# Optimization experiments

Measured on AMD Instinct MI355X. Metric: run time of the kernel, lower is better.

Reference implementation:

```python
import jax, jax.numpy as jnp
import numpy as np

NEG_INF = -1e30


def setup_inputs() -> dict:
    key = jax.random.key(0)
    ks = jax.random.split(key, 11)
    b, n, d = 4, 2048, 1024
    scale = 1.0 / np.sqrt(d)
    inp = {
        "q": jax.random.normal(ks[0], (b, n, d), jnp.float32),
        "k": jax.random.normal(ks[1], (b, n, d), jnp.float32),
        "v": jax.random.normal(ks[2], (b, n, d), jnp.float32),
        # nn.Linear params: weight [out, in], bias [out]
        "Wq": jax.random.normal(ks[3], (d, d), jnp.float32) * scale,
        "bq": jnp.zeros((d,), jnp.float32),
        "Wk": jax.random.normal(ks[4], (d, d), jnp.float32) * scale,
        "bk": jnp.zeros((d,), jnp.float32),
        "Wv": jax.random.normal(ks[5], (d, d), jnp.float32) * scale,
        "bv": jnp.zeros((d,), jnp.float32),
        "Wo": jax.random.normal(ks[6], (d, d), jnp.float32) * scale,
        "bo": jnp.zeros((d,), jnp.float32),
    }
    return inp


def reference(q, k, v, Wq, bq, Wk, bk, Wv, bv, Wo, bo):
    # Faithful to source: the multi-head reshape/transpose results are never
    # assigned, so attention runs single-headed over full n_embd vectors.
    b, n, d = q.shape
    qp = q @ Wq.T + bq  # [b, n, d]
    kp = k @ Wk.T + bk
    vp = v @ Wv.T + bv
    scale = jnp.asarray(1.0 / d, qp.dtype) ** 0.5  # sqrt(1/d)
    att = jnp.einsum('bnd,bmd->bnm', qp, kp) * scale  # [b, n, n]
    causal = jnp.tril(jnp.ones((n, n), bool))          # block_size tril sliced to n
    att = jnp.where(causal[None, :, :], att, NEG_INF)
    att = jax.nn.softmax(att, axis=-1)  # dropout p=0.0 -> identity
    y = att @ vp                        # [b, n, d]
    # source bug reproduced: transpose(1,2) then reshape(b, n, d)
    y = jnp.swapaxes(y, 1, 2).reshape(b, n, d)
    y = y @ Wo.T + bo
    return y
```

## Files before the change

### kernel.cpp

```cpp
#include <hip/hip_runtime.h>
#include <hip/hip_bf16.h>
#include <stdint.h>

typedef __bf16 bf16_t;
typedef __bf16 bf16x8 __attribute__((ext_vector_type(8)));
typedef __bf16 bf16x4 __attribute__((ext_vector_type(4)));
typedef float f32x4 __attribute__((ext_vector_type(4)));

#define GLD_LDS16(src, dst)                                                              \
  __builtin_amdgcn_global_load_lds((const __attribute__((address_space(1))) void*)(src), \
                                   (__attribute__((address_space(3))) void*)(dst), 16, 0, 0)

struct CvtArgs {
  const float* src[7];
  bf16_t* dst[7];
  long n4[7];
};

__global__ __launch_bounds__(256) void cvt_all(CvtArgs a) {
  const int seg = blockIdx.y;
  const float* __restrict__ in = a.src[seg];
  bf16_t* __restrict__ out = a.dst[seg];
  const long n4 = a.n4[seg];
  long i = (long)blockIdx.x * blockDim.x + threadIdx.x;
  const long stride = (long)gridDim.x * blockDim.x;
  for (; i < n4; i += stride) {
    float4 v = ((const float4*)in)[i];
    bf16x4 o;
    o[0] = (bf16_t)v.x; o[1] = (bf16_t)v.y; o[2] = (bf16_t)v.z; o[3] = (bf16_t)v.w;
    ((bf16x4*)out)[i] = o;
  }
}

__global__ __launch_bounds__(256) void softmax_causal(bf16_t* __restrict__ S, int n, long sB) {
  const int i = blockIdx.x;
  const int z = blockIdx.y;
  bf16_t* row = S + (long)z * sB + (long)i * n;
  const int t = threadIdx.x;
  const int j0 = t << 3;
  const int jmax = ((i >> 7) + 1) << 7;
  const bool active = j0 < jmax;

  float vals[8];
  float mx = -3.0e38f;
  if (active) {
    bf16x8 vv = ((const bf16x8*)row)[t];
#pragma unroll
    for (int e = 0; e < 8; ++e) {
      float v = (j0 + e <= i) ? (float)vv[e] : -3.0e38f;
      vals[e] = v;
      mx = fmaxf(mx, v);
    }
  }
#pragma unroll
  for (int off = 32; off; off >>= 1) mx = fmaxf(mx, __shfl_xor(mx, off));
  __shared__ float redm[4];
  if ((t & 63) == 0) redm[t >> 6] = mx;
  __syncthreads();
  mx = fmaxf(fmaxf(redm[0], redm[1]), fmaxf(redm[2], redm[3]));

  float sum = 0.f;
  if (active) {
#pragma unroll
    for (int e = 0; e < 8; ++e) {
      float p = (j0 + e <= i) ? __expf(vals[e] - mx) : 0.f;
      vals[e] = p;
      sum += p;
    }
  }
#pragma unroll
  for (int off = 32; off; off >>= 1) sum += __shfl_xor(sum, off);
  __shared__ float reds[4];
  if ((t & 63) == 0) reds[t >> 6] = sum;
  __syncthreads();
  sum = reds[0] + reds[1] + reds[2] + reds[3];
  const float inv = 1.0f / sum;

  if (active) {
    bf16x8 o;
#pragma unroll
    for (int e = 0; e < 8; ++e) o[e] = (bf16_t)(vals[e] * inv);
    ((bf16x8*)row)[t] = o;
  }
}

__device__ __forceinline__ void xcd_remap(int& bx, int& by, int& bz) {
  const int gx = gridDim.x, gy = gridDim.y;
  int lin = (blockIdx.z * gy + blockIdx.y) * gx + blockIdx.x;
  const int nwg = gx * gy * (int)gridDim.z;
  lin = (lin & 7) * (nwg >> 3) + (lin >> 3);
  bx = lin % gx;
  const int rem = lin / gx;
  by = rem % gy;
  bz = rem / gy;
}

template <int NF>
__device__ __forceinline__ void gemm_core(char* smem,
                                          const bf16_t* __restrict__ A,
                                          const bf16_t* __restrict__ B,
                                          int K, int KT, int m0, int n0,
                                          f32x4 (&acc)[4][NF]) {
  char* const asb = smem;
  char* const bsb = smem + 16384;
  const int t = threadIdx.x;
  const int l = t & 63;
  const int w = t >> 6;
  const int wr = w >> 1, wc = w & 1;
  const int r16 = l & 15, kg = l >> 4;

  const bf16_t* a_src[4];
  const bf16_t* b_src[NF];
#pragma unroll
  for (int i = 0; i < 4; ++i) {
    const int c = i * 256 + t;
    const int row = c >> 3;
    const int sl = (c & 7) ^ (row & 7);
    a_src[i] = A + (long)(m0 + row) * K + sl * 8;
  }
#pragma unroll
  for (int i = 0; i < NF; ++i) {
    const int c = i * 256 + t;
    const int row = c >> 3;
    const int sl = (c & 7) ^ (row & 7);
    b_src[i] = B + (long)(n0 + row) * K + sl * 8;
  }

  int aoff[2][4], boff[2][NF];
#pragma unroll
  for (int kp = 0; kp < 2; ++kp) {
#pragma unroll
    for (int mi = 0; mi < 4; ++mi) {
      const int ra = wr * 64 + mi * 16 + r16;
      aoff[kp][mi] = ra * 128 + ((kp * 4 + kg) ^ (ra & 7)) * 16;
    }
#pragma unroll
    for (int ni = 0; ni < NF; ++ni) {
      const int rb = wc * (NF * 16) + ni * 16 + r16;
      boff[kp][ni] = rb * 128 + ((kp * 4 + kg) ^ (rb & 7)) * 16;
    }
  }

  for (int kt = 0; kt < KT; ++kt) {
    __syncthreads();
#pragma unroll
    for (int i = 0; i < 4; ++i) {
      GLD_LDS16(a_src[i], asb + i * 4096 + w * 1024);
      a_src[i] += 64;
    }
#pragma unroll
    for (int i = 0; i < NF; ++i) {
      GLD_LDS16(b_src[i], bsb + i * 4096 + w * 1024);
      b_src[i] += 64;
    }
    __syncthreads();

#pragma unroll
    for (int kp = 0; kp < 2; ++kp) {
      bf16x8 af[4], bfr[NF];
#pragma unroll
      for (int mi = 0; mi < 4; ++mi) af[mi] = *(const bf16x8*)(asb + aoff[kp][mi]);
#pragma unroll
      for (int ni = 0; ni < NF; ++ni) bfr[ni] = *(const bf16x8*)(bsb + boff[kp][ni]);
#pragma unroll
      for (int mi = 0; mi < 4; ++mi)
#pragma unroll
        for (int ni = 0; ni < NF; ++ni)
          acc[mi][ni] =
              __builtin_amdgcn_mfma_f32_16x16x32_bf16(af[mi], bfr[ni], acc[mi][ni], 0, 0, 0);
    }
  }
}

template <int NF, int EPI, bool BIAS, bool KBOUND>
__global__ __launch_bounds__(256, 4) void gemm_bt(const bf16_t* __restrict__ Ag,
                                                  const bf16_t* __restrict__ Bg,
                                                  const float* __restrict__ bias,
                                                  void* __restrict__ Cout,
                                                  int N, int K, float alpha,
                                                  long sAb, long sBb, long sCb, int eltC) {
  int bx, by, bz;
  xcd_remap(bx, by, bz);
  const int m0 = by << 7, n0 = bx * (NF * 32);

  int KT = K >> 6;
  if (KBOUND) {
    const int kb = (n0 + NF * 32) >> 6;
    if (kb < KT) KT = kb;
  }

  __shared__ __align__(16) char smem[16384 + NF * 4096];
  f32x4 acc[4][NF] = {};
  gemm_core<NF>(smem, Ag + (long)bz * sAb, Bg + (long)bz * sBb, K, KT, m0, n0, acc);

  const int t = threadIdx.x;
  const int l = t & 63;
  const int w = t >> 6;
  const int wr = w >> 1, wc = w & 1;
  const int rowbase = m0 + wr * 64 + ((l >> 4) << 2);
  const int colbase = n0 + wc * (NF * 16) + (l & 15);
  if constexpr (EPI == 0) {
    float* C = (float*)((char*)Cout + (long)bz * sCb * eltC);
#pragma unroll
    for (int mi = 0; mi < 4; ++mi)
#pragma unroll
      for (int ni = 0; ni < NF; ++ni) {
        const int col = colbase + ni * 16;
        float badd = 0.f;
        if constexpr (BIAS) badd = bias[col];
#pragma unroll
        for (int j = 0; j < 4; ++j)
          C[(long)(rowbase + mi * 16 + j) * N + col] = acc[mi][ni][j] * alpha + badd;
      }
  } else {
    bf16_t* C = (bf16_t*)((char*)Cout + (long)bz * sCb * eltC);
#pragma unroll
    for (int mi = 0; mi < 4; ++mi)
#pragma unroll
      for (int ni = 0; ni < NF; ++ni) {
        const int col = colbase + ni * 16;
        float badd = 0.f;
        if constexpr (BIAS) badd = bias[col];
#pragma unroll
        for (int j = 0; j < 4; ++j)
          C[(long)(rowbase + mi * 16 + j) * N + col] = (bf16_t)(acc[mi][ni][j] * alpha + badd);
      }
  }
}

__global__ __launch_bounds__(256, 4) void gemm_scores(const bf16_t* __restrict__ qp,
                                                      const bf16_t* __restrict__ kp,
                                                      bf16_t* __restrict__ S,
                                                      long nd, long nn) {
  int bx, by, bz;
  xcd_remap(bx, by, bz);
  int r, c;
  if (bx <= 2 * by + 1) { r = by; c = bx; }
  else { r = 15 - by; c = bx + 15 - 2 * by; }
  const int m0 = r << 7, n0 = c << 6;

  __shared__ __align__(16) char smem[24576];
  f32x4 acc[4][2] = {};
  gemm_core<2>(smem, qp + (long)bz * nd, kp + (long)bz * nd, 1024, 16, m0, n0, acc);

  const int t = threadIdx.x;
  const int l = t & 63;
  const int w = t >> 6;
  const int wr = w >> 1, wc = w & 1;
  const int rowbase = m0 + wr * 64 + ((l >> 4) << 2);
  const int colbase = n0 + wc * 32 + (l & 15);
  bf16_t* C = S + (long)bz * nn;
#pragma unroll
  for (int mi = 0; mi < 4; ++mi)
#pragma unroll
    for (int ni = 0; ni < 2; ++ni) {
      const int col = colbase + ni * 16;
#pragma unroll
      for (int j = 0; j < 4; ++j)
        C[(long)(rowbase + mi * 16 + j) * 2048 + col] = (bf16_t)(acc[mi][ni][j] * 0.03125f);
    }
}

struct Qkv3Args {
  const bf16_t* A[3];
  const bf16_t* W[3];
  const float* bias[3];
  bf16_t* C[3];
};

__global__ __launch_bounds__(256, 4) void qkv3(Qkv3Args ga, int N, int K) {
  int bx, by, bz;
  xcd_remap(bx, by, bz);
  const int m0 = by << 7, n0 = bx << 7;

  __shared__ __align__(16) char smem[32768];
  f32x4 acc[4][4] = {};
  gemm_core<4>(smem, ga.A[bz], ga.W[bz], K, K >> 6, m0, n0, acc);

  const float* __restrict__ bias = ga.bias[bz];
  const int t = threadIdx.x;
  const int l = t & 63;
  const int w = t >> 6;
  const int wr = w >> 1, wc = w & 1;
  const int r16 = l & 15, kg = l >> 4;

  if (bz < 2) {
    bf16_t* C = ga.C[bz];
    const int rowbase = m0 + wr * 64 + kg * 4;
    const int colbase = n0 + wc * 64 + r16;
#pragma unroll
    for (int mi = 0; mi < 4; ++mi)
#pragma unroll
      for (int ni = 0; ni < 4; ++ni) {
        const int col = colbase + ni * 16;
        const float badd = bias[col];
#pragma unroll
        for (int j = 0; j < 4; ++j)
          C[(long)(rowbase + mi * 16 + j) * N + col] = (bf16_t)(acc[mi][ni][j] + badd);
      }
  } else {
    __syncthreads();
    char* tt = smem;
#pragma unroll
    for (int mi = 0; mi < 4; ++mi)
#pragma unroll
      for (int ni = 0; ni < 4; ++ni) {
        const int lc = wc * 64 + ni * 16 + r16;
        const int lrb = (wr * 64 + mi * 16 + kg * 4) * 2;
        const float badd = bias[n0 + lc];
        bf16x4 o;
#pragma unroll
        for (int j = 0; j < 4; ++j) o[j] = (bf16_t)(acc[mi][ni][j] + badd);
        *(bf16x4*)(tt + lc * 256 + (lrb ^ ((lc & 7) << 4))) = o;
      }
    __syncthreads();
    bf16_t* C = ga.C[2];
    const int batch = m0 >> 11, nb = m0 & 2047;
#pragma unroll
    for (int i = 0; i < 8; ++i) {
      const int c = i * 256 + t;
      const int lc = c >> 4, ch = c & 15;
      *(bf16x8*)(C + (long)batch * (2048 * 1024) + (long)(n0 + lc) * 2048 + nb + ch * 8) =
          *(const bf16x8*)(tt + lc * 256 + ((ch * 16) ^ ((lc & 7) << 4)));
    }
  }
}

extern "C" void kernel_launch(void* const* d_in, const int* in_sizes, int n_in,
                              void* d_out, int out_size, void* d_ws, size_t ws_size,
                              hipStream_t stream) {
  const int b = 4, n = 2048, d = 1024;
  const long nd  = (long)n * d;
  const long bn  = (long)b * n;
  const long bnd = bn * d;
  const long ddl = (long)d * d;
  const long nn  = (long)n * n;

  const float* q  = (const float*)d_in[0];
  const float* k  = (const float*)d_in[1];
  const float* v  = (const float*)d_in[2];
  const float* Wq = (const float*)d_in[3];
  const float* bq = (const float*)d_in[4];
  const float* Wk = (const float*)d_in[5];
  const float* bk = (const float*)d_in[6];
  const float* Wv = (const float*)d_in[7];
  const float* bv = (const float*)d_in[8];
  const float* Wo = (const float*)d_in[9];
  const float* bo = (const float*)d_in[10];

  bf16_t* ws  = (bf16_t*)d_ws;
  bf16_t* qB  = ws;
  bf16_t* kB  = qB + bnd;
  bf16_t* vB  = kB + bnd;
  bf16_t* WqB = vB + bnd;
  bf16_t* WkB = WqB + ddl;
  bf16_t* WvB = WkB + ddl;
  bf16_t* WoB = WvB + ddl;
  bf16_t* qpB = WoB + ddl;
  bf16_t* kpB = qpB + bnd;
  bf16_t* vpT = kpB + bnd;
  bf16_t* S   = vpT + bnd;
  bf16_t* yT  = S + (long)b * nn;
  const size_t need = (size_t)(7 * bnd + 4 * ddl + (long)b * nn) * 2;
  if (ws_size < need) return;

  dim3 blk(256);

  CvtArgs ca;
  ca.src[0] = q;  ca.dst[0] = qB;  ca.n4[0] = bnd / 4;
  ca.src[1] = k;  ca.dst[1] = kB;  ca.n4[1] = bnd / 4;
  ca.src[2] = v;  ca.dst[2] = vB;  ca.n4[2] = bnd / 4;
  ca.src[3] = Wq; ca.dst[3] = WqB; ca.n4[3] = ddl / 4;
  ca.src[4] = Wk; ca.dst[4] = WkB; ca.n4[4] = ddl / 4;
  ca.src[5] = Wv; ca.dst[5] = WvB; ca.n4[5] = ddl / 4;
  ca.src[6] = Wo; ca.dst[6] = WoB; ca.n4[6] = ddl / 4;
  cvt_all<<<dim3(512, 7), blk, 0, stream>>>(ca);

  Qkv3Args qa;
  qa.A[0] = qB; qa.W[0] = WqB; qa.bias[0] = bq; qa.C[0] = qpB;
  qa.A[1] = kB; qa.W[1] = WkB; qa.bias[1] = bk; qa.C[1] = kpB;
  qa.A[2] = vB; qa.W[2] = WvB; qa.bias[2] = bv; qa.C[2] = vpT;
  qkv3<<<dim3(d / 128, bn / 128, 3), blk, 0, stream>>>(qa, d, d);

  gemm_scores<<<dim3(17, 16, b), blk, 0, stream>>>(qpB, kpB, S, nd, nn);

  softmax_causal<<<dim3(n, b), blk, 0, stream>>>(S, n, nn);

  gemm_bt<2, 1, false, true><<<dim3(n / 64, d / 128, b), blk, 0, stream>>>(
      vpT, S, nullptr, yT, n, n, 1.f, nd, nn, nd, 2);

  gemm_bt<2, 0, true, false><<<dim3(d / 64, bn / 128, 1), blk, 0, stream>>>(
      yT, WoB, bo, (float*)d_out, d, d, 1.f, 0, 0, 0, 4);
}
```

Baseline: 181.3 us.

## Switch GEMM core from 16x16x32 to 32x32x16 bf16 MFMA tiles

Reworks the shared GEMM core and every epilogue to use 32x32x16 MFMA instructions with 16-wide f32 accumulators in place of 16x16x32 with 4-wide ones. Tile sizes per block stay the same but fragment offsets, LDS read patterns and output index mapping are rewritten. Larger MFMA tiles need fewer LDS fragment reads per FLOP and fewer instructions issued. The cost is longer per-instruction latency, a different register-pressure profile, and a write pattern where each lane stores rows spaced 8 apart.

```diff
diff --git a/kernel.cpp b/kernel.cpp
--- a/kernel.cpp
+++ b/kernel.cpp
@@ -6,6 +6,7 @@
 typedef __bf16 bf16x8 __attribute__((ext_vector_type(8)));
 typedef __bf16 bf16x4 __attribute__((ext_vector_type(4)));
 typedef float f32x4 __attribute__((ext_vector_type(4)));
+typedef float f32x16 __attribute__((ext_vector_type(16)));
 
 #define GLD_LDS16(src, dst)                                                              \
   __builtin_amdgcn_global_load_lds((const __attribute__((address_space(1))) void*)(src), \
@@ -95,22 +96,22 @@
   bz = rem / gy;
 }
 
-template <int NF>
+template <int NS>
 __device__ __forceinline__ void gemm_core(char* smem,
                                           const bf16_t* __restrict__ A,
                                           const bf16_t* __restrict__ B,
                                           int K, int KT, int m0, int n0,
-                                          f32x4 (&acc)[4][NF]) {
+                                          f32x16 (&acc)[2][NS]) {
   char* const asb = smem;
   char* const bsb = smem + 16384;
   const int t = threadIdx.x;
   const int l = t & 63;
   const int w = t >> 6;
   const int wr = w >> 1, wc = w & 1;
-  const int r16 = l & 15, kg = l >> 4;
+  const int l31 = l & 31, hi = l >> 5;
 
   const bf16_t* a_src[4];
-  const bf16_t* b_src[NF];
+  const bf16_t* b_src[NS * 2];
 #pragma unroll
   for (int i = 0; i < 4; ++i) {
     const int c = i * 256 + t;
@@ -119,25 +120,25 @@
     a_src[i] = A + (long)(m0 + row) * K + sl * 8;
   }
 #pragma unroll
-  for (int i = 0; i < NF; ++i) {
+  for (int i = 0; i < NS * 2; ++i) {
     const int c = i * 256 + t;
     const int row = c >> 3;
     const int sl = (c & 7) ^ (row & 7);
     b_src[i] = B + (long)(n0 + row) * K + sl * 8;
   }
 
-  int aoff[2][4], boff[2][NF];
-#pragma unroll
-  for (int kp = 0; kp < 2; ++kp) {
-#pragma unroll
-    for (int mi = 0; mi < 4; ++mi) {
-      const int ra = wr * 64 + mi * 16 + r16;
-      aoff[kp][mi] = ra * 128 + ((kp * 4 + kg) ^ (ra & 7)) * 16;
-    }
-#pragma unroll
-    for (int ni = 0; ni < NF; ++ni) {
-      const int rb = wc * (NF * 16) + ni * 16 + r16;
-      boff[kp][ni] = rb * 128 + ((kp * 4 + kg) ^ (rb & 7)) * 16;
+  int aoff[4][2], boff[4][NS];
+#pragma unroll
+  for (int kt = 0; kt < 4; ++kt) {
+#pragma unroll
+    for (int mi = 0; mi < 2; ++mi) {
+      const int ra = wr * 64 + mi * 32 + l31;
+      aoff[kt][mi] = ra * 128 + ((kt * 2 + hi) ^ (ra & 7)) * 16;
+    }
+#pragma unroll
+    for (int ni = 0; ni < NS; ++ni) {
+      const int rb = wc * (NS * 32) + ni * 32 + l31;
+      boff[kt][ni] = rb * 128 + ((kt * 2 + hi) ^ (rb & 7)) * 16;
     }
   }
 
@@ -149,30 +150,30 @@
       a_src[i] += 64;
     }
 #pragma unroll
-    for (int i = 0; i < NF; ++i) {
+    for (int i = 0; i < NS * 2; ++i) {
       GLD_LDS16(b_src[i], bsb + i * 4096 + w * 1024);
       b_src[i] += 64;
     }
     __syncthreads();
 
 #pragma unroll
-    for (int kp = 0; kp < 2; ++kp) {
-      bf16x8 af[4], bfr[NF];
-#pragma unroll
-      for (int mi = 0; mi < 4; ++mi) af[mi] = *(const bf16x8*)(asb + aoff[kp][mi]);
-#pragma unroll
-      for (int ni = 0; ni < NF; ++ni) bfr[ni] = *(const bf16x8*)(bsb + boff[kp][ni]);
-#pragma unroll
-      for (int mi = 0; mi < 4; ++mi)
-#pragma unroll
-        for (int ni = 0; ni < NF; ++ni)
+    for (int ks = 0; ks < 4; ++ks) {
+      bf16x8 af[2], bfr[NS];
+#pragma unroll
+      for (int mi = 0; mi < 2; ++mi) af[mi] = *(const bf16x8*)(asb + aoff[ks][mi]);
+#pragma unroll
+      for (int ni = 0; ni < NS; ++ni) bfr[ni] = *(const bf16x8*)(bsb + boff[ks][ni]);
+#pragma unroll
+      for (int mi = 0; mi < 2; ++mi)
+#pragma unroll
+        for (int ni = 0; ni < NS; ++ni)
           acc[mi][ni] =
-              __builtin_amdgcn_mfma_f32_16x16x32_bf16(af[mi], bfr[ni], acc[mi][ni], 0, 0, 0);
-    }
-  }
-}
-
-template <int NF, int EPI, bool BIAS, bool KBOUND>
+              __builtin_amdgcn_mfma_f32_32x32x16_bf16(af[mi], bfr[ni], acc[mi][ni], 0, 0, 0);
+    }
+  }
+}
+
+template <int NS, int EPI, bool BIAS, bool KBOUND>
 __global__ __launch_bounds__(256, 4) void gemm_bt(const bf16_t* __restrict__ Ag,
                                                   const bf16_t* __restrict__ Bg,
                                                   const float* __restrict__ bias,
@@ -181,49 +182,56 @@
                                                   long sAb, long sBb, long sCb, int eltC) {
   int bx, by, bz;
   xcd_remap(bx, by, bz);
-  const int m0 = by << 7, n0 = bx * (NF * 32);
+  const int m0 = by << 7, n0 = bx * (NS * 64);
 
   int KT = K >> 6;
   if (KBOUND) {
-    const int kb = (n0 + NF * 32) >> 6;
+    const int kb = (n0 + NS * 64) >> 6;
     if (kb < KT) KT = kb;
   }
 
-  __shared__ __align__(16) char smem[16384 + NF * 4096];
-  f32x4 acc[4][NF] = {};
-  gemm_core<NF>(smem, Ag + (long)bz * sAb, Bg + (long)bz * sBb, K, KT, m0, n0, acc);
+  __shared__ __align__(16) char smem[16384 + NS * 8192];
+  f32x16 acc[2][NS] = {};
+  gemm_core<NS>(smem, Ag + (long)bz * sAb, Bg + (long)bz * sBb, K, KT, m0, n0, acc);
 
   const int t = threadIdx.x;
   const int l = t & 63;
   const int w = t >> 6;
   const int wr = w >> 1, wc = w & 1;
-  const int rowbase = m0 + wr * 64 + ((l >> 4) << 2);
-  const int colbase = n0 + wc * (NF * 16) + (l & 15);
+  const int l31 = l & 31, hi = l >> 5;
   if constexpr (EPI == 0) {
     float* C = (float*)((char*)Cout + (long)bz * sCb * eltC);
 #pragma unroll
-    for (int mi = 0; mi < 4; ++mi)
-#pragma unroll
-      for (int ni = 0; ni < NF; ++ni) {
-        const int col = colbase + ni * 16;
+    for (int mi = 0; mi < 2; ++mi)
+#pragma unroll
+      for (int ni = 0; ni < NS; ++ni) {
+        const int col = n0 + wc * (NS * 32) + ni * 32 + l31;
         float badd = 0.f;
         if constexpr (BIAS) badd = bias[col];
 #pragma unroll
-        for (int j = 0; j < 4; ++j)
-          C[(long)(rowbase + mi * 16 + j) * N + col] = acc[mi][ni][j] * alpha + badd;
+        for (int g = 0; g < 4; ++g)
+#pragma unroll
+          for (int j = 0; j < 4; ++j) {
+            const int row = m0 + wr * 64 + mi * 32 + hi * 4 + g * 8 + j;
+            C[(long)row * N + col] = acc[mi][ni][g * 4 + j] * alpha + badd;
+          }
       }
   } else {
     bf16_t* C = (bf16_t*)((char*)Cout + (long)bz * sCb * eltC);
 #pragma unroll
-    for (int mi = 0; mi < 4; ++mi)
-#pragma unroll
-      for (int ni = 0; ni < NF; ++ni) {
-        const int col = colbase + ni * 16;
+    for (int mi = 0; mi < 2; ++mi)
+#pragma unroll
+      for (int ni = 0; ni < NS; ++ni) {
+        const int col = n0 + wc * (NS * 32) + ni * 32 + l31;
         float badd = 0.f;
         if constexpr (BIAS) badd = bias[col];
 #pragma unroll
-        for (int j = 0; j < 4; ++j)
-          C[(long)(rowbase + mi * 16 + j) * N + col] = (bf16_t)(acc[mi][ni][j] * alpha + badd);
+        for (int g = 0; g < 4; ++g)
+#pragma unroll
+          for (int j = 0; j < 4; ++j) {
+            const int row = m0 + wr * 64 + mi * 32 + hi * 4 + g * 8 + j;
+            C[(long)row * N + col] = (bf16_t)(acc[mi][ni][g * 4 + j] * alpha + badd);
+          }
       }
   }
 }
@@ -240,25 +248,26 @@
   const int m0 = r << 7, n0 = c << 6;
 
   __shared__ __align__(16) char smem[24576];
-  f32x4 acc[4][2] = {};
-  gemm_core<2>(smem, qp + (long)bz * nd, kp + (long)bz * nd, 1024, 16, m0, n0, acc);
+  f32x16 acc[2][1] = {};
+  gemm_core<1>(smem, qp + (long)bz * nd, kp + (long)bz * nd, 1024, 16, m0, n0, acc);
 
   const int t = threadIdx.x;
   const int l = t & 63;
   const int w = t >> 6;
   const int wr = w >> 1, wc = w & 1;
-  const int rowbase = m0 + wr * 64 + ((l >> 4) << 2);
-  const int colbase = n0 + wc * 32 + (l & 15);
+  const int l31 = l & 31, hi = l >> 5;
   bf16_t* C = S + (long)bz * nn;
 #pragma unroll
-  for (int mi = 0; mi < 4; ++mi)
-#pragma unroll
-    for (int ni = 0; ni < 2; ++ni) {
-      const int col = colbase + ni * 16;
-#pragma unroll
-      for (int j = 0; j < 4; ++j)
-        C[(long)(rowbase + mi * 16 + j) * 2048 + col] = (bf16_t)(acc[mi][ni][j] * 0.03125f);
-    }
+  for (int mi = 0; mi < 2; ++mi) {
+    const int col = n0 + wc * 32 + l31;
+#pragma unroll
+    for (int g = 0; g < 4; ++g)
+#pragma unroll
+      for (int j = 0; j < 4; ++j) {
+        const int row = m0 + wr * 64 + mi * 32 + hi * 4 + g * 8 + j;
+        C[(long)row * 2048 + col] = (bf16_t)(acc[mi][0][g * 4 + j] * 0.03125f);
+      }
+  }
 }
 
 struct Qkv3Args {
@@ -274,44 +283,50 @@
   const int m0 = by << 7, n0 = bx << 7;
 
   __shared__ __align__(16) char smem[32768];
-  f32x4 acc[4][4] = {};
-  gemm_core<4>(smem, ga.A[bz], ga.W[bz], K, K >> 6, m0, n0, acc);
+  f32x16 acc[2][2] = {};
+  gemm_core<2>(smem, ga.A[bz], ga.W[bz], K, K >> 6, m0, n0, acc);
 
   const float* __restrict__ bias = ga.bias[bz];
   const int t = threadIdx.x;
   const int l = t & 63;
   const int w = t >> 6;
   const int wr = w >> 1, wc = w & 1;
-  const int r16 = l & 15, kg = l >> 4;
+  const int l31 = l & 31, hi = l >> 5;
 
   if (bz < 2) {
     bf16_t* C = ga.C[bz];
-    const int rowbase = m0 + wr * 64 + kg * 4;
-    const int colbase = n0 + wc * 64 + r16;
-#pragma unroll
-    for (int mi = 0; mi < 4; ++mi)
-#pragma unroll
-      for (int ni = 0; ni < 4; ++ni) {
-        const int col = colbase + ni * 16;
+#pragma unroll
+    for (int mi = 0; mi < 2; ++mi)
+#pragma unroll
+      for (int ni = 0; ni < 2; ++ni) {
+        const int col = n0 + wc * 64 + ni * 32 + l31;
         const float badd = bias[col];
 #pragma unroll
-        for (int j = 0; j < 4; ++j)
-          C[(long)(rowbase + mi * 16 + j) * N + col] = (bf16_t)(acc[mi][ni][j] + badd);
+        for (int g = 0; g < 4; ++g)
+#pragma unroll
+          for (int j = 0; j < 4; ++j) {
+            const int row = m0 + wr * 64 + mi * 32 + hi * 4 + g * 8 + j;
+            C[(long)row * N + col] = (bf16_t)(acc[mi][ni][g * 4 + j] + badd);
+          }
       }
   } else {
     __syncthreads();
     char* tt = smem;
 #pragma unroll
-    for (int mi = 0; mi < 4; ++mi)
-#pragma unroll
-      for (int ni = 0; ni < 4; ++ni) {
-        const int lc = wc * 64 + ni * 16 + r16;
-        const int lrb = (wr * 64 + mi * 16 + kg * 4) * 2;
+    for (int mi = 0; mi < 2; ++mi)
+#pragma unroll
+      for (int ni = 0; ni < 2; ++ni) {
+        const int lc = wc * 64 + ni * 32 + l31;
         const float badd = bias[n0 + lc];
-        bf16x4 o;
-#pragma unroll
-        for (int j = 0; j < 4; ++j) o[j] = (bf16_t)(acc[mi][ni][j] + badd);
-        *(bf16x4*)(tt + lc * 256 + (lrb ^ ((lc & 7) << 4))) = o;
+#pragma unroll
+        for (int g = 0; g < 4; ++g) {
+          const int lr = wr * 64 + mi * 32 + hi * 4 + g * 8;
+          const int lrb = lr * 2;
+          bf16x4 o;
+#pragma unroll
+          for (int j = 0; j < 4; ++j) o[j] = (bf16_t)(acc[mi][ni][g * 4 + j] + badd);
+          *(bf16x4*)(tt + lc * 256 + (lrb ^ ((lc & 7) << 4))) = o;
+        }
       }
     __syncthreads();
     bf16_t* C = ga.C[2];
@@ -386,9 +401,9 @@
 
   softmax_causal<<<dim3(n, b), blk, 0, stream>>>(S, n, nn);
 
-  gemm_bt<2, 1, false, true><<<dim3(n / 64, d / 128, b), blk, 0, stream>>>(
+  gemm_bt<1, 1, false, true><<<dim3(n / 64, d / 128, b), blk, 0, stream>>>(
       vpT, S, nullptr, yT, n, n, 1.f, nd, nn, nd, 2);
 
-  gemm_bt<2, 0, true, false><<<dim3(d / 64, bn / 128, 1), blk, 0, stream>>>(
+  gemm_bt<1, 0, true, false><<<dim3(d / 64, bn / 128, 1), blk, 0, stream>>>(
       yT, WoB, bo, (float*)d_out, d, d, 1.f, 0, 0, 0, 4);
 }
```

Result: slower. 193.9 us (+7.0%).
